# Kernel optimization log

Measured on AMD Instinct MI355X. Metric: run time of the kernel, lower is better.

The kernel has to match this reference:

```python
import jax, jax.numpy as jnp
import numpy as np

H, KVH, D = 8, 4, 256
SCALING = 256.0 ** -0.5   # query_pre_attn_scalar ** -0.5
SOFTCAP = 50.0
THETA = 10000.0
WINDOW = 1024


def setup_inputs() -> dict:
    key = jax.random.key(0)
    ks = jax.random.split(key, 5)
    B, S, HID = 2, 2048, 2304
    return {
        "hidden_states": jax.random.normal(ks[0], (B, S, HID), jnp.float32),
        "Wq": jax.random.normal(ks[1], (H * D, HID), jnp.float32) * 0.02,
        "Wk": jax.random.normal(ks[2], (KVH * D, HID), jnp.float32) * 0.02,
        "Wv": jax.random.normal(ks[3], (KVH * D, HID), jnp.float32) * 0.02,
        "Wo": jax.random.normal(ks[4], (HID, H * D), jnp.float32) * 0.02,
        "position_ids": jnp.arange(S, dtype=jnp.int32),
    }


def _rotate_half(x):
    x1, x2 = x[..., : D // 2], x[..., D // 2 :]
    return jnp.concatenate((-x2, x1), axis=-1)


def reference(hidden_states, Wq, Wk, Wv, Wo, position_ids):
    B, S, HID = hidden_states.shape
    # projections (torch Linear: y = x @ W.T)
    q = (hidden_states @ Wq.T).reshape(B, S, H, D).transpose(0, 2, 1, 3)      # [B,H,S,D]
    k = (hidden_states @ Wk.T).reshape(B, S, KVH, D).transpose(0, 2, 1, 3)    # [B,KVH,S,D]
    v = (hidden_states @ Wv.T).reshape(B, S, KVH, D).transpose(0, 2, 1, 3)

    # rotary embedding
    inv_freq = 1.0 / (THETA ** (jnp.arange(0, D, 2, dtype=jnp.float32) / D))  # [D/2]
    freqs = position_ids.astype(jnp.float32)[:, None] * inv_freq[None, :]     # [S,D/2]
    emb = jnp.concatenate((freqs, freqs), axis=-1)                            # [S,D]
    cos = jnp.cos(emb)[None, None]                                            # [1,1,S,D]
    sin = jnp.sin(emb)[None, None]
    q = q * cos + _rotate_half(q) * sin
    k = k * cos + _rotate_half(k) * sin

    # repeat_kv (GQA)
    n_rep = H // KVH
    k = jnp.repeat(k, n_rep, axis=1)  # [B,H,S,D]
    v = jnp.repeat(v, n_rep, axis=1)

    # softcapped attention scores
    scores = jnp.einsum("bhqd,bhkd->bhqk", q, k) * SCALING
    scores = SOFTCAP * jnp.tanh(scores / SOFTCAP)

    # causal + sliding-window mask
    i = jnp.arange(S)[:, None]
    j = jnp.arange(S)[None, :]
    allowed = (j <= i) & (i - j < WINDOW)
    scores = jnp.where(allowed[None, None], scores, jnp.finfo(scores.dtype).min)

    attn = jax.nn.softmax(scores.astype(jnp.float32), axis=-1).astype(q.dtype)
    out = jnp.einsum("bhqk,bhkd->bhqd", attn, v)          # [B,H,S,D]
    out = out.transpose(0, 2, 1, 3).reshape(B, S, H * D)   # [B,S,H*D]
    return out @ Wo.T                                      # [B,S,HID]
```

## Files before the change

### kernel.cpp

```cpp
#include <hip/hip_runtime.h>

typedef _Float16 half8 __attribute__((ext_vector_type(8)));
typedef _Float16 half4v __attribute__((ext_vector_type(4)));
typedef float floatx4 __attribute__((ext_vector_type(4)));
typedef float floatx16 __attribute__((ext_vector_type(16)));

#define GLD16(g, l) __builtin_amdgcn_global_load_lds(                          \
    (__attribute__((address_space(1))) void*)(g),                              \
    (__attribute__((address_space(3))) void*)(l), 16, 0, 0)

__global__ void cvt_all(const float* __restrict__ s0, const float* __restrict__ s1,
                        const float* __restrict__ s2, const float* __restrict__ s3,
                        const float* __restrict__ s4, _Float16* __restrict__ d0,
                        _Float16* __restrict__ d1, _Float16* __restrict__ d2,
                        _Float16* __restrict__ d3, _Float16* __restrict__ d4) {
  long i = (long)blockIdx.x * 256 + threadIdx.x;
  const float* s;
  _Float16* d;
  long off;
  if (i < 2359296) { s = s0; d = d0; off = i; }
  else if (i < 3538944) { s = s1; d = d1; off = i - 2359296; }
  else if (i < 4128768) { s = s2; d = d2; off = i - 3538944; }
  else if (i < 4718592) { s = s3; d = d3; off = i - 4128768; }
  else { s = s4; d = d4; off = i - 4718592; }
  const float4 v = *(const float4*)(s + off * 4);
  half4v o = {(_Float16)v.x, (_Float16)v.y, (_Float16)v.z, (_Float16)v.w};
  *(half4v*)(d + off * 4) = o;
}

template <typename TO>
__global__ __launch_bounds__(256) void gemm_nt(const _Float16* __restrict__ A,
                                               const _Float16* __restrict__ B,
                                               TO* __restrict__ C, int M, int N,
                                               int K) {
  __shared__ __align__(16) _Float16 lA[2][128 * 64];
  __shared__ __align__(16) _Float16 lB[2][128 * 64];
  const int tid = threadIdx.x;
  const int lane = tid & 63;
  const int w = tid >> 6;
  const int wm = w >> 1, wn = w & 1;
  const int l31 = lane & 31;
  const int kg = lane >> 5;
  const long tM = (long)blockIdx.y * 128;
  const long tN = (long)blockIdx.x * 128;

  floatx16 acc[2][2] = {};

  const _Float16* Ab = A + tM * K;
  const _Float16* Bb = B + tN * K;

  int sr[4], sc_[4];
#pragma unroll
  for (int p = 0; p < 4; ++p) {
    const int U = p * 256 + tid;
    sr[p] = U >> 3;
    sc_[p] = ((U & 7) ^ (sr[p] & 7)) << 3;
  }

#pragma unroll
  for (int p = 0; p < 4; ++p) {
    const int U = p * 256 + tid;
    GLD16(Ab + (long)sr[p] * K + sc_[p], &lA[0][U * 8]);
    GLD16(Bb + (long)sr[p] * K + sc_[p], &lB[0][U * 8]);
  }

  int cur = 0;
  for (int k0 = 0; k0 < K; k0 += 64) {
    __syncthreads();
    if (k0 + 64 < K) {
      const int nxt = cur ^ 1;
#pragma unroll
      for (int p = 0; p < 4; ++p) {
        const int U = p * 256 + tid;
        GLD16(Ab + (long)sr[p] * K + (k0 + 64 + sc_[p]), &lA[nxt][U * 8]);
        GLD16(Bb + (long)sr[p] * K + (k0 + 64 + sc_[p]), &lB[nxt][U * 8]);
      }
    }
#pragma unroll
    for (int t = 0; t < 4; ++t) {
      const int g = t * 2 + kg;
      half8 af[2], bf[2];
#pragma unroll
      for (int i = 0; i < 2; ++i) {
        const int ra = wm * 64 + i * 32 + l31;
        af[i] = *(const half8*)&lA[cur][ra * 64 + ((g ^ (ra & 7)) << 3)];
      }
#pragma unroll
      for (int j = 0; j < 2; ++j) {
        const int rb = wn * 64 + j * 32 + l31;
        bf[j] = *(const half8*)&lB[cur][rb * 64 + ((g ^ (rb & 7)) << 3)];
      }
#pragma unroll
      for (int i = 0; i < 2; ++i)
#pragma unroll
        for (int j = 0; j < 2; ++j)
          acc[i][j] = __builtin_amdgcn_mfma_f32_32x32x16_f16(af[i], bf[j],
                                                             acc[i][j], 0, 0, 0);
    }
    cur ^= 1;
  }

#pragma unroll
  for (int i = 0; i < 2; ++i)
#pragma unroll
    for (int j = 0; j < 2; ++j) {
      const long col = tN + wn * 64 + j * 32 + l31;
#pragma unroll
      for (int reg = 0; reg < 16; ++reg) {
        const long row =
            tM + wm * 64 + i * 32 + (reg & 3) + 8 * (reg >> 2) + 4 * kg;
        C[row * N + col] = (TO)acc[i][j][reg];
      }
    }
}

__global__ void rope_qk(const _Float16* __restrict__ QKV,
                        const int* __restrict__ pos_ids,
                        _Float16* __restrict__ Qr, _Float16* __restrict__ Kr) {
  const int idx = blockIdx.x * blockDim.x + threadIdx.x;
  const int d = idx & 127;
  const int rest = idx >> 7;
  const int head = rest % 12;
  const int ms = rest / 12;
  const int s = ms & 2047;
  const int b = ms >> 11;
  const float ang = (float)pos_ids[s] * expf(d * -0.07195578164f);
  const float c = cosf(ang), sn = sinf(ang);
  if (head < 8) {
    const _Float16* src = QKV + (long)ms * 4096 + head * 256 + d;
    const float x1 = (float)src[0], x2 = (float)src[128];
    _Float16* dst = Qr + (((long)b * 8 + head) * 2048 + s) * 256 + d;
    dst[0] = (_Float16)(x1 * c - x2 * sn);
    dst[128] = (_Float16)(x2 * c + x1 * sn);
  } else {
    const int kh = head - 8;
    const _Float16* src = QKV + (long)ms * 4096 + 2048 + kh * 256 + d;
    const float x1 = (float)src[0], x2 = (float)src[128];
    _Float16* dst = Kr + (((long)b * 4 + kh) * 2048 + s) * 256 + d;
    dst[0] = (_Float16)(x1 * c - x2 * sn);
    dst[128] = (_Float16)(x2 * c + x1 * sn);
  }
}

__global__ void vtrans(const _Float16* __restrict__ QKV,
                       _Float16* __restrict__ Vt) {
  __shared__ _Float16 lT[64 * 65];
  const int tid = threadIdx.x;
  const int ss = blockIdx.x * 64;
  const int dd = blockIdx.y * 64;
  const int z = blockIdx.z;
  const int b = z >> 2, kvh = z & 3;

#pragma unroll
  for (int pass = 0; pass < 2; ++pass) {
    const int U = pass * 256 + tid;
    const int s_loc = U >> 3, du = U & 7;
    const half8 v = *(const half8*)(QKV + ((long)(b * 2048 + ss + s_loc)) * 4096 +
                                    3072 + kvh * 256 + dd + du * 8);
#pragma unroll
    for (int e = 0; e < 8; ++e) lT[s_loc * 65 + du * 8 + e] = v[e];
  }
  __syncthreads();
#pragma unroll
  for (int pass = 0; pass < 2; ++pass) {
    const int U = pass * 256 + tid;
    const int su = U & 7, dl = (U >> 3) & 63;
    half8 o;
#pragma unroll
    for (int e = 0; e < 8; ++e) o[e] = lT[(su * 8 + e) * 65 + dl];
    *(half8*)(Vt + ((long)z * 256 + dd + dl) * 2048 + ss + su * 8) = o;
  }
}

__global__ __launch_bounds__(256, 2) void attn_fwd(
    const _Float16* __restrict__ Q, const _Float16* __restrict__ K,
    const _Float16* __restrict__ Vt, _Float16* __restrict__ AO) {
  __shared__ __align__(16) _Float16 lK[2][64 * 256];
  __shared__ __align__(16) _Float16 lP[64 * 76];

  const int tid = threadIdx.x;
  const int lane = tid & 63;
  const int w = tid >> 6;
  const int quad = lane >> 4, l15 = lane & 15;

  const int qt = blockIdx.x;
  const int h = blockIdx.y;
  const int b = blockIdx.z;
  const int kvh = h >> 1;
  const int qs = qt * 64;

  const _Float16* Qb = Q + (((long)b * 8 + h) * 2048) * 256;
  const _Float16* Kb = K + (((long)b * 4 + kvh) * 2048) * 256;
  const _Float16* Vb = Vt + (((long)b * 4 + kvh) * 256) * 2048;

  half8 qf[8];
  {
    const _Float16* qp = Qb + (long)(qs + w * 16 + l15) * 256 + quad * 8;
#pragma unroll
    for (int t = 0; t < 8; ++t) qf[t] = *(const half8*)(qp + t * 32);
  }
  half8 onesv;
#pragma unroll
  for (int e = 0; e < 8; ++e) onesv[e] = (_Float16)1.f;

  floatx4 o[4][4] = {};
  floatx4 lacc[4] = {};

  const int kt_lo = qt >= 16 ? qt - 16 : 0;

  {
    const _Float16* kt0 = Kb + (long)kt_lo * 64 * 256;
#pragma unroll
    for (int p = 0; p < 8; ++p) {
      const int U = p * 256 + tid;
      const int r = U >> 5, u = U & 31;
      GLD16(kt0 + r * 256 + ((u ^ (r & 7)) << 3), &lK[0][U * 8]);
    }
  }

  int cur = 0;
  for (int kt = kt_lo; kt <= qt; ++kt, cur ^= 1) {
    const int ks = kt * 64;
    __syncthreads();

    half8 vf[2][4];
#pragma unroll
    for (int t2 = 0; t2 < 2; ++t2)
#pragma unroll
      for (int j = 0; j < 4; ++j) {
        const int d = w * 64 + j * 16 + l15;
        vf[t2][j] = *(const half8*)(Vb + (long)d * 2048 + ks + t2 * 32 + quad * 8);
      }
    if (kt < qt) {
      const _Float16* kt0 = Kb + (long)(ks + 64) * 256;
      const int nxt = cur ^ 1;
#pragma unroll
      for (int p = 0; p < 8; ++p) {
        const int U = p * 256 + tid;
        const int r = U >> 5, u = U & 31;
        GLD16(kt0 + r * 256 + ((u ^ (r & 7)) << 3), &lK[nxt][U * 8]);
      }
    }

    floatx4 sc[4] = {};
#pragma unroll
    for (int t = 0; t < 8; ++t)
#pragma unroll
      for (int j = 0; j < 4; ++j) {
        const half8 kf = *(const half8*)&lK[cur][(j * 16 + l15) * 256 +
                                                 (((t * 4 + quad) ^ (l15 & 7)) << 3)];
        sc[j] = __builtin_amdgcn_mfma_f32_16x16x32_f16(qf[t], kf, sc[j], 0, 0, 0);
      }

    const bool need_mask = (kt == qt) || (kt == qt - 16);
    const int qr0 = qs + w * 16 + quad * 4;
#pragma unroll
    for (int j = 0; j < 4; ++j) {
      const int key = ks + j * 16 + l15;
#pragma unroll
      for (int r = 0; r < 4; ++r) {
        const float s = sc[j][r] * 0.0625f;
        const float t2 = (s * 0.02f) * (s * 0.02f);
        const float cap = s * (1.f + t2 * (-0.33333333f + t2 * 0.13333333f));
        float p = __expf(cap - 5.f);
        if (need_mask) {
          const bool ok = (key <= qr0 + r) && (qr0 + r - key < 1024);
          p = ok ? p : 0.f;
        }
        lP[(w * 16 + quad * 4 + r) * 76 + j * 16 + l15] = (_Float16)p;
      }
    }
    __syncthreads();

#pragma unroll
    for (int t2 = 0; t2 < 2; ++t2) {
      half8 pf[4];
#pragma unroll
      for (int i = 0; i < 4; ++i)
        pf[i] = *(const half8*)&lP[(i * 16 + l15) * 76 + t2 * 32 + quad * 8];
#pragma unroll
      for (int i = 0; i < 4; ++i) {
        lacc[i] = __builtin_amdgcn_mfma_f32_16x16x32_f16(pf[i], onesv, lacc[i],
                                                         0, 0, 0);
#pragma unroll
        for (int j = 0; j < 4; ++j)
          o[i][j] = __builtin_amdgcn_mfma_f32_16x16x32_f16(pf[i], vf[t2][j],
                                                           o[i][j], 0, 0, 0);
      }
    }
  }

  _Float16* aop = AO + ((long)b * 2048 + qs) * 2048 + (long)h * 256;
#pragma unroll
  for (int i = 0; i < 4; ++i)
#pragma unroll
    for (int r = 0; r < 4; ++r) {
      const int row = i * 16 + quad * 4 + r;
      const float inv = 1.0f / lacc[i][r];
#pragma unroll
      for (int j = 0; j < 4; ++j)
        aop[(long)row * 2048 + w * 64 + j * 16 + l15] =
            (_Float16)(o[i][j][r] * inv);
    }
}

extern "C" void kernel_launch(void* const* d_in, const int* in_sizes, int n_in,
                              void* d_out, int out_size, void* d_ws,
                              size_t ws_size, hipStream_t stream) {
  const float* hs = (const float*)d_in[0];
  const float* Wq = (const float*)d_in[1];
  const float* Wk = (const float*)d_in[2];
  const float* Wv = (const float*)d_in[3];
  const float* Wo = (const float*)d_in[4];
  const int* pos = (const int*)d_in[5];
  float* out = (float*)d_out;

  _Float16* Xf = (_Float16*)d_ws;
  _Float16* Wqkv = Xf + 4096L * 2304;
  _Float16* Wo16 = Wqkv + 4096L * 2304;
  _Float16* QKV = Wo16 + 2304L * 2048;
  _Float16* Qr = QKV + 4096L * 4096;
  _Float16* Kr = Qr + 2L * 8 * 2048 * 256;
  _Float16* Vt = Kr + 2L * 4 * 2048 * 256;
  _Float16* AO = Xf;

  cvt_all<<<dim3(23040), dim3(256), 0, stream>>>(
      hs, Wq, Wk, Wv, Wo, Xf, Wqkv, Wqkv + 2048L * 2304, Wqkv + 3072L * 2304,
      Wo16);

  gemm_nt<_Float16><<<dim3(32, 32), dim3(256), 0, stream>>>(Xf, Wqkv, QKV, 4096,
                                                            4096, 2304);
  rope_qk<<<dim3(2 * 2048 * 12 * 128 / 256), dim3(256), 0, stream>>>(QKV, pos,
                                                                     Qr, Kr);
  vtrans<<<dim3(32, 4, 8), dim3(256), 0, stream>>>(QKV, Vt);
  attn_fwd<<<dim3(32, 8, 2), dim3(256), 0, stream>>>(Qr, Kr, Vt, AO);
  gemm_nt<float><<<dim3(18, 32), dim3(256), 0, stream>>>(AO, Wo16, out, 4096,
                                                         2304, 2048);
}
```

Measured before the change: 379.8 us.

## Replace 128x128 GEMM with 256x256 ping-pong pipelined MFMA GEMM

Swaps the 128x128 double-buffered GEMM for a 256x256-tile, 512-thread kernel. It stages global-to-LDS loads in half-tile chunks interleaved with 16x16x32 MFMA phases, using explicit vmcnt waits, barriers and setprio. It also remaps workgroup IDs to improve L2 locality. The aim is more operand reuse and better overlap of memory with compute in both the QKV and output projections, at the cost of fewer workgroups (256 and 144 blocks). Correctness relies on the hand-placed waitcnt and barrier ordering, and on K being a multiple of 128.

Measured after the change: 358.8 us. 5.5% less time.

```diff
diff --git a/kernel.cpp b/kernel.cpp
--- a/kernel.cpp
+++ b/kernel.cpp
@@ -3,11 +3,13 @@
 typedef _Float16 half8 __attribute__((ext_vector_type(8)));
 typedef _Float16 half4v __attribute__((ext_vector_type(4)));
 typedef float floatx4 __attribute__((ext_vector_type(4)));
-typedef float floatx16 __attribute__((ext_vector_type(16)));
 
 #define GLD16(g, l) __builtin_amdgcn_global_load_lds(                          \
     (__attribute__((address_space(1))) void*)(g),                              \
     (__attribute__((address_space(3))) void*)(l), 16, 0, 0)
+
+#define VM4 asm volatile("s_waitcnt vmcnt(4)" ::: "memory")
+#define VM0 asm volatile("s_waitcnt vmcnt(0)" ::: "memory")
 
 __global__ void cvt_all(const float* __restrict__ s0, const float* __restrict__ s1,
                         const float* __restrict__ s2, const float* __restrict__ s3,
@@ -28,90 +30,125 @@
   *(half4v*)(d + off * 4) = o;
 }
 
+__device__ __forceinline__ void stg_half(const _Float16* __restrict__ g,
+                                         _Float16* l, int h, long k0, int K,
+                                         int tid, const long* gofs) {
+#pragma unroll
+  for (int p = 0; p < 2; ++p)
+    GLD16(g + (long)h * 128 * K + k0 + gofs[p],
+          l + (h * 1024 + p * 512 + tid) * 8);
+}
+
+#define LDB(buf)                                                               \
+  _Pragma("unroll") for (int n = 0; n < 4; ++n)                                \
+  _Pragma("unroll") for (int ks = 0; ks < 2; ++ks)                             \
+      bfr[n][ks] = *(const half8*)&lB[buf][boff0 + n * 1024 +                  \
+                                           (((ks * 4 + quad) ^ xq) << 3)];
+
+#define PH(buf, q, VMW, ...)                                                   \
+  {                                                                            \
+    half8 af[2][2];                                                            \
+    _Pragma("unroll") for (int m2 = 0; m2 < 2; ++m2)                           \
+    _Pragma("unroll") for (int ks = 0; ks < 2; ++ks)                           \
+        af[m2][ks] = *(const half8*)&lA[buf][aoff0 + ((q) * 2 + m2) * 1024 +   \
+                                             (((ks * 4 + quad) ^ xq) << 3)];   \
+    __VA_ARGS__;                                                               \
+    __builtin_amdgcn_sched_barrier(0);                                         \
+    __builtin_amdgcn_s_barrier();                                              \
+    __builtin_amdgcn_sched_barrier(0);                                         \
+    __builtin_amdgcn_s_setprio(1);                                             \
+    _Pragma("unroll") for (int ks = 0; ks < 2; ++ks)                           \
+    _Pragma("unroll") for (int m2 = 0; m2 < 2; ++m2)                           \
+    _Pragma("unroll") for (int n = 0; n < 4; ++n)                              \
+        acc[(q) * 2 + m2][n] = __builtin_amdgcn_mfma_f32_16x16x32_f16(         \
+            af[m2][ks], bfr[n][ks], acc[(q) * 2 + m2][n], 0, 0, 0);            \
+    __builtin_amdgcn_s_setprio(0);                                             \
+    VMW;                                                                       \
+    __builtin_amdgcn_sched_barrier(0);                                         \
+    __builtin_amdgcn_s_barrier();                                              \
+    __builtin_amdgcn_sched_barrier(0);                                         \
+  }
+
 template <typename TO>
-__global__ __launch_bounds__(256) void gemm_nt(const _Float16* __restrict__ A,
-                                               const _Float16* __restrict__ B,
-                                               TO* __restrict__ C, int M, int N,
-                                               int K) {
-  __shared__ __align__(16) _Float16 lA[2][128 * 64];
-  __shared__ __align__(16) _Float16 lB[2][128 * 64];
+__global__ __launch_bounds__(512, 2) void gemm256(
+    const _Float16* __restrict__ A, const _Float16* __restrict__ B,
+    TO* __restrict__ C, int M, int N, int K) {
+  __shared__ __align__(16) _Float16 lA[2][16384];
+  __shared__ __align__(16) _Float16 lB[2][16384];
   const int tid = threadIdx.x;
   const int lane = tid & 63;
   const int w = tid >> 6;
-  const int wm = w >> 1, wn = w & 1;
-  const int l31 = lane & 31;
-  const int kg = lane >> 5;
-  const long tM = (long)blockIdx.y * 128;
-  const long tN = (long)blockIdx.x * 128;
-
-  floatx16 acc[2][2] = {};
+  const int wm = w >> 2, wn = w & 3;
+  const int quad = lane >> 4, l15 = lane & 15;
+  const int xq = l15 & 7;
+
+  const int nwg = gridDim.x * gridDim.y;
+  int wg = blockIdx.y * gridDim.x + blockIdx.x;
+  if (!(nwg & 7)) wg = (wg & 7) * (nwg >> 3) + (wg >> 3);
+  const int bx = wg % gridDim.x, by = wg / gridDim.x;
+  const long tM = (long)by * 256, tN = (long)bx * 256;
 
   const _Float16* Ab = A + tM * K;
   const _Float16* Bb = B + tN * K;
 
-  int sr[4], sc_[4];
-#pragma unroll
-  for (int p = 0; p < 4; ++p) {
-    const int U = p * 256 + tid;
-    sr[p] = U >> 3;
-    sc_[p] = ((U & 7) ^ (sr[p] & 7)) << 3;
-  }
-
-#pragma unroll
-  for (int p = 0; p < 4; ++p) {
-    const int U = p * 256 + tid;
-    GLD16(Ab + (long)sr[p] * K + sc_[p], &lA[0][U * 8]);
-    GLD16(Bb + (long)sr[p] * K + sc_[p], &lB[0][U * 8]);
-  }
-
-  int cur = 0;
-  for (int k0 = 0; k0 < K; k0 += 64) {
-    __syncthreads();
-    if (k0 + 64 < K) {
-      const int nxt = cur ^ 1;
-#pragma unroll
-      for (int p = 0; p < 4; ++p) {
-        const int U = p * 256 + tid;
-        GLD16(Ab + (long)sr[p] * K + (k0 + 64 + sc_[p]), &lA[nxt][U * 8]);
-        GLD16(Bb + (long)sr[p] * K + (k0 + 64 + sc_[p]), &lB[nxt][U * 8]);
-      }
-    }
-#pragma unroll
-    for (int t = 0; t < 4; ++t) {
-      const int g = t * 2 + kg;
-      half8 af[2], bf[2];
-#pragma unroll
-      for (int i = 0; i < 2; ++i) {
-        const int ra = wm * 64 + i * 32 + l31;
-        af[i] = *(const half8*)&lA[cur][ra * 64 + ((g ^ (ra & 7)) << 3)];
-      }
-#pragma unroll
-      for (int j = 0; j < 2; ++j) {
-        const int rb = wn * 64 + j * 32 + l31;
-        bf[j] = *(const half8*)&lB[cur][rb * 64 + ((g ^ (rb & 7)) << 3)];
-      }
-#pragma unroll
-      for (int i = 0; i < 2; ++i)
-#pragma unroll
-        for (int j = 0; j < 2; ++j)
-          acc[i][j] = __builtin_amdgcn_mfma_f32_32x32x16_f16(af[i], bf[j],
-                                                             acc[i][j], 0, 0, 0);
-    }
-    cur ^= 1;
-  }
-
-#pragma unroll
-  for (int i = 0; i < 2; ++i)
-#pragma unroll
-    for (int j = 0; j < 2; ++j) {
-      const long col = tN + wn * 64 + j * 32 + l31;
-#pragma unroll
-      for (int reg = 0; reg < 16; ++reg) {
-        const long row =
-            tM + wm * 64 + i * 32 + (reg & 3) + 8 * (reg >> 2) + 4 * kg;
-        C[row * N + col] = (TO)acc[i][j][reg];
-      }
-    }
+  long gofs[2];
+#pragma unroll
+  for (int p = 0; p < 2; ++p) {
+    const int U = p * 512 + tid;
+    const int r = U >> 3;
+    gofs[p] = (long)r * K + (((U & 7) ^ (r & 7)) << 3);
+  }
+
+  const int aoff0 = (wm * 128 + l15) * 64;
+  const int boff0 = (wn * 64 + l15) * 64;
+
+  floatx4 acc[8][4] = {};
+  half8 bfr[4][2];
+
+  stg_half(Bb, &lB[0][0], 0, 0, K, tid, gofs);
+  stg_half(Bb, &lB[0][0], 1, 0, K, tid, gofs);
+  stg_half(Ab, &lA[0][0], 0, 0, K, tid, gofs);
+  stg_half(Ab, &lA[0][0], 1, 0, K, tid, gofs);
+  stg_half(Bb, &lB[1][0], 0, 64, K, tid, gofs);
+  stg_half(Bb, &lB[1][0], 1, 64, K, tid, gofs);
+  VM4;
+  __builtin_amdgcn_sched_barrier(0);
+  __builtin_amdgcn_s_barrier();
+  __builtin_amdgcn_sched_barrier(0);
+
+  const int NI = K >> 7;
+  for (int i = 0; i < NI; ++i) {
+    const long ks0 = (long)i << 7;
+    const bool fin = (i == NI - 1);
+    LDB(0);
+    PH(0, 0, (void)0, stg_half(Ab, &lA[1][0], 0, ks0 + 64, K, tid, gofs));
+    PH(0, 1, (void)0, stg_half(Ab, &lA[1][0], 1, ks0 + 64, K, tid, gofs));
+    PH(0, 2, (void)0,
+       if (!fin) stg_half(Bb, &lB[0][0], 0, ks0 + 128, K, tid, gofs));
+    PH(0, 3, if (fin) { VM0; } else { VM4; },
+       if (!fin) stg_half(Bb, &lB[0][0], 1, ks0 + 128, K, tid, gofs));
+    LDB(1);
+    PH(1, 0, (void)0,
+       if (!fin) stg_half(Ab, &lA[0][0], 0, ks0 + 128, K, tid, gofs));
+    PH(1, 1, (void)0,
+       if (!fin) stg_half(Ab, &lA[0][0], 1, ks0 + 128, K, tid, gofs));
+    PH(1, 2, (void)0,
+       if (!fin) stg_half(Bb, &lB[1][0], 0, ks0 + 192, K, tid, gofs));
+    PH(1, 3, if (!fin) { VM4; },
+       if (!fin) stg_half(Bb, &lB[1][0], 1, ks0 + 192, K, tid, gofs));
+  }
+
+#pragma unroll
+  for (int m = 0; m < 8; ++m) {
+#pragma unroll
+    for (int n = 0; n < 4; ++n) {
+      const long col = tN + wn * 64 + n * 16 + l15;
+      const long row0 = tM + wm * 128 + m * 16 + quad * 4;
+#pragma unroll
+      for (int r = 0; r < 4; ++r)
+        C[(row0 + r) * N + col] = (TO)acc[m][n][r];
+    }
+  }
 }
 
 __global__ void rope_qk(const _Float16* __restrict__ QKV,
@@ -328,12 +365,12 @@
       hs, Wq, Wk, Wv, Wo, Xf, Wqkv, Wqkv + 2048L * 2304, Wqkv + 3072L * 2304,
       Wo16);
 
-  gemm_nt<_Float16><<<dim3(32, 32), dim3(256), 0, stream>>>(Xf, Wqkv, QKV, 4096,
-                                                            4096, 2304);
+  gemm256<_Float16><<<dim3(16, 16), dim3(512), 0, stream>>>(Xf, Wqkv, QKV,
+                                                            4096, 4096, 2304);
   rope_qk<<<dim3(2 * 2048 * 12 * 128 / 256), dim3(256), 0, stream>>>(QKV, pos,
                                                                      Qr, Kr);
   vtrans<<<dim3(32, 4, 8), dim3(256), 0, stream>>>(QKV, Vt);
   attn_fwd<<<dim3(32, 8, 2), dim3(256), 0, stream>>>(Qr, Kr, Vt, AO);
-  gemm_nt<float><<<dim3(18, 32), dim3(256), 0, stream>>>(AO, Wo16, out, 4096,
-                                                         2304, 2048);
-}
+  gemm256<float><<<dim3(9, 16), dim3(512), 0, stream>>>(AO, Wo16, out, 4096,
+                                                        2304, 2048);
+}
```
